# Kernel optimization log

Hardware: AMD Instinct MI355X
Metric: run time of the kernel (lower is better)

The kernel has to match this reference:

```python
import jax, jax.numpy as jnp
import numpy as np
from jax import lax

RADIUS = 51  # radius=50 bumped to odd in __init__
# cv2.getGaussianKernel(51, 0): sigma = 0.3*((ksize-1)*0.5 - 1) + 0.8 = 8.0
SIGMA = 0.3 * ((RADIUS - 1) * 0.5 - 1) + 0.8
WEIGHT = 0.5
THRESHOLD = 10.0


def _gaussian_kernel2d():
    x = np.arange(RADIUS, dtype=np.float64) - (RADIUS - 1) / 2.0
    g = np.exp(-(x ** 2) / (2.0 * SIGMA ** 2))
    g = g / g.sum()
    k2d = np.outer(g, g)
    return jnp.asarray(k2d, dtype=jnp.float32)


def filter2d(img, kernel):
    # img: (b, h, w, c); kernel: (k, k); reflect pad + depthwise conv, VALID
    k = kernel.shape[-1]
    c = img.shape[-1]
    p = k // 2
    imgp = jnp.pad(img, [(0, 0), (p, p), (p, p), (0, 0)], mode='reflect')
    kern = jnp.tile(kernel[:, :, None, None].astype(img.dtype), (1, 1, 1, c))  # HWIO, I=1
    return lax.conv_general_dilated(
        imgp, kern, window_strides=(1, 1), padding='VALID',
        dimension_numbers=('NHWC', 'HWIO', 'NHWC'), feature_group_count=c)


def setup_inputs() -> dict:
    key = jax.random.key(0)
    img = jax.random.uniform(key, (16, 512, 512, 3), dtype=jnp.float32)
    kernel = _gaussian_kernel2d()
    return {"img": img, "kernel": kernel}


def reference(img, kernel):
    blur = filter2d(img, kernel)
    residual = img - blur
    mask = (jnp.abs(residual) * 255.0 > THRESHOLD).astype(img.dtype)
    soft_mask = filter2d(mask, kernel)
    sharp = jnp.clip(img + WEIGHT * residual, 0.0, 1.0)
    return soft_mask * sharp + (1.0 - soft_mask) * img
```

## Files before the change

### kernel.cpp

```cpp
#include <hip/hip_runtime.h>
#include <hip/hip_fp16.h>

#define BB 16
#define HH 512
#define ROWLEN 1536
#define KK 51
#define RR 25

__device__ __forceinline__ int sq(int q) { return q ^ ((q >> 3) & 7); }

__global__ void k_weights(const float* __restrict__ k2d, float* __restrict__ g,
                          __half2* __restrict__ g2) {
    int i = threadIdx.x;
    if (i < KK) {
        float s = 0.f;
        for (int j = 0; j < KK; ++j) s += k2d[i * KK + j];
        g[i] = s;
        g2[i] = __float2half2_rn(s);
    }
}

#define PSTR 576
template<bool U8>
__global__ __launch_bounds__(256, 4) void k_hconv(const void* __restrict__ srcv,
                                                  __half* __restrict__ dst,
                                                  __half* __restrict__ imgh,
                                                  const __half2* __restrict__ g2src) {
    __shared__ __align__(16) __half2 pl[6 * PSTR];
    const int t = threadIdx.x;
    const int row0 = blockIdx.x * 4;

    __half2 gw2[KK];
    #pragma unroll
    for (int i = 0; i < KK; ++i) gw2[i] = g2src[i];

    const int rp = t >> 7;
    const int l  = t & 127;
    const size_t rb0 = (size_t)(row0 + 2 * rp) * ROWLEN;
    const size_t rb1 = rb0 + ROWLEN;

    {
        float f0[12], f1[12];
        if (U8) {
            const unsigned char* sa = (const unsigned char*)srcv + rb0 + 12 * l;
            const unsigned char* sb = (const unsigned char*)srcv + rb1 + 12 * l;
            unsigned int wa[3], wb[3];
            wa[0] = *(const unsigned int*)(sa);
            wa[1] = *(const unsigned int*)(sa + 4);
            wa[2] = *(const unsigned int*)(sa + 8);
            wb[0] = *(const unsigned int*)(sb);
            wb[1] = *(const unsigned int*)(sb + 4);
            wb[2] = *(const unsigned int*)(sb + 8);
            #pragma unroll
            for (int k = 0; k < 12; ++k) {
                f0[k] = (float)((wa[k >> 2] >> ((k & 3) * 8)) & 0xffu);
                f1[k] = (float)((wb[k >> 2] >> ((k & 3) * 8)) & 0xffu);
            }
        } else {
            const float* sfa = (const float*)srcv + rb0 + 12 * l;
            const float* sfb = (const float*)srcv + rb1 + 12 * l;
            *(float4*)&f0[0] = *(const float4*)(sfa);
            *(float4*)&f0[4] = *(const float4*)(sfa + 4);
            *(float4*)&f0[8] = *(const float4*)(sfa + 8);
            *(float4*)&f1[0] = *(const float4*)(sfb);
            *(float4*)&f1[4] = *(const float4*)(sfb + 4);
            *(float4*)&f1[8] = *(const float4*)(sfb + 8);
            union { __half h[12]; uint2 u2[3]; } pa, pb2;
            #pragma unroll
            for (int k = 0; k < 12; ++k) {
                pa.h[k]  = __float2half_rn(f0[k]);
                pb2.h[k] = __float2half_rn(f1[k]);
            }
            uint2* ipa = (uint2*)(imgh + rb0 + 12 * l);
            uint2* ipb = (uint2*)(imgh + rb1 + 12 * l);
            ipa[0] = pa.u2[0];  ipa[1] = pa.u2[1];  ipa[2] = pa.u2[2];
            ipb[0] = pb2.u2[0]; ipb[1] = pb2.u2[1]; ipb[2] = pb2.u2[2];
        }
        const int q = sq(7 + l);
        #pragma unroll
        for (int c = 0; c < 3; ++c) {
            union { __half2 h2[4]; uint4 u; } o;
            #pragma unroll
            for (int i = 0; i < 4; ++i)
                o.h2[i] = __halves2half2(__float2half_rn(f0[3 * i + c]),
                                         __float2half_rn(f1[3 * i + c]));
            *(uint4*)&pl[(rp * 3 + c) * PSTR + 4 * q] = o.u;
        }
    }
    __syncthreads();

    #pragma unroll
    for (int it = 0; it < 2; ++it) {
        const int item = t + it * 256;
        if (item < 300) {
            const int p = item / 50, k = item % 50;
            int ed, es;
            if (k < 25) { const int j = k + 1;  ed = 28 - j;  es = 28 + j; }
            else        { const int j = k - 24; ed = 539 + j; es = 539 - j; }
            __half2* pb = &pl[p * PSTR];
            pb[4 * sq(ed >> 2) + (ed & 3)] = pb[4 * sq(es >> 2) + (es & 3)];
        }
    }
    __syncthreads();

    __half2 acc2[3][4];
    const __half2 z2 = __float2half2_rn(0.f);
    #pragma unroll
    for (int c = 0; c < 3; ++c)
        #pragma unroll
        for (int a = 0; a < 4; ++a) acc2[c][a] = z2;

    #pragma unroll
    for (int c = 0; c < 3; ++c) {
        const __half2* pb = &pl[(rp * 3 + c) * PSTR];
        #pragma unroll
        for (int v = 0; v < 15; ++v) {
            union { uint4 u; __half2 h2[4]; } v4;
            v4.u = *(const uint4*)&pb[4 * sq(l + v)];
            #pragma unroll
            for (int mm = 0; mm < 4; ++mm) {
                const __half2 val = v4.h2[mm];
                #pragma unroll
                for (int a = 0; a < 4; ++a) {
                    const int jj = 4 * v + mm - a - 3;
                    if (jj >= 0 && jj < KK)
                        acc2[c][a] = __hfma2(gw2[jj], val, acc2[c][a]);
                }
            }
        }
    }

    {
        union { __half h[12]; uint2 u2[3]; } pk;
        #pragma unroll
        for (int a = 0; a < 4; ++a)
            #pragma unroll
            for (int c = 0; c < 3; ++c) pk.h[3 * a + c] = __low2half(acc2[c][a]);
        uint2* dp = (uint2*)(dst + rb0 + 12 * l);
        dp[0] = pk.u2[0]; dp[1] = pk.u2[1]; dp[2] = pk.u2[2];
    }
    {
        union { __half h[12]; uint2 u2[3]; } pk;
        #pragma unroll
        for (int a = 0; a < 4; ++a)
            #pragma unroll
            for (int c = 0; c < 3; ++c) pk.h[3 * a + c] = __high2half(acc2[c][a]);
        uint2* dp = (uint2*)(dst + rb1 + 12 * l);
        dp[0] = pk.u2[0]; dp[1] = pk.u2[1]; dp[2] = pk.u2[2];
    }
}

#define HC 128
#define VROWS 178
#define HSTR 72

template<int MODE>
__global__ __launch_bounds__(256) void k_vconv(const __half* __restrict__ src,
                                               const __half* __restrict__ imgh,
                                               __half* __restrict__ sharp16,
                                               float* __restrict__ outp,
                                               unsigned char* __restrict__ mask8,
                                               const __half2* __restrict__ g2src) {
    __shared__ __align__(16) __half tile[VROWS * HSTR];
    const int t  = threadIdx.x;
    const int cg = t & 7;
    const int rg = t >> 3;
    const int bid = blockIdx.x;
    const int wcB = bid % 24;
    const int hB  = (bid / 24) & 3;
    const int b   = bid / 96;
    const int wc0 = wcB * 64;
    const int h0  = hB * HC;

    __half2 gw2[KK];
    #pragma unroll
    for (int i = 0; i < KK; ++i) gw2[i] = g2src[i];

    const size_t imgbase = (size_t)b * HH * ROWLEN;

    #pragma unroll
    for (int i = 0; i < 6; ++i) {
        const int m = t + 256 * i;
        if (m < VROWS * 8) {
            const int r = m >> 3, cc = m & 7;
            int hs = h0 - RR + r;
            hs = hs < 0 ? -hs : hs;
            hs = hs > 511 ? 1022 - hs : hs;
            *(uint4*)&tile[r * HSTR + 8 * cc] =
                *(const uint4*)&src[imgbase + (size_t)hs * ROWLEN + wc0 + 8 * cc];
        }
    }
    __syncthreads();

    __half2 acc[4][4];
    const __half2 z2 = __float2half2_rn(0.f);
    #pragma unroll
    for (int a = 0; a < 4; ++a)
        #pragma unroll
        for (int p = 0; p < 4; ++p) acc[a][p] = z2;

    const __half* base = &tile[(rg * 4) * HSTR + 8 * cg];
    #pragma unroll
    for (int jj = 0; jj < 54; ++jj) {
        const uint4 raw = *(const uint4*)(base + jj * HSTR);
        union { uint4 u; __half2 h2[4]; } v; v.u = raw;
        #pragma unroll
        for (int a = 0; a < 4; ++a) {
            const int tap = jj - a;
            if (tap >= 0 && tap < KK) {
                acc[a][0] = __hfma2(gw2[tap], v.h2[0], acc[a][0]);
                acc[a][1] = __hfma2(gw2[tap], v.h2[1], acc[a][1]);
                acc[a][2] = __hfma2(gw2[tap], v.h2[2], acc[a][2]);
                acc[a][3] = __hfma2(gw2[tap], v.h2[3], acc[a][3]);
            }
        }
    }

    #pragma unroll
    for (int a = 0; a < 4; ++a) {
        const int hh = h0 + rg * 4 + a;
        const size_t idx = imgbase + (size_t)hh * ROWLEN + wc0 + 8 * cg;
        union { uint4 u; __half2 h2[4]; } xl;
        xl.u = *(const uint4*)&imgh[idx];
        float xv[8], bv[8];
        #pragma unroll
        for (int p = 0; p < 4; ++p) {
            const float2 xf = __half22float2(xl.h2[p]);
            const float2 bf = __half22float2(acc[a][p]);
            xv[2*p] = xf.x; xv[2*p+1] = xf.y;
            bv[2*p] = bf.x; bv[2*p+1] = bf.y;
        }
        if (MODE == 0) {
            union { __half h[8]; uint4 u; } sh;
            unsigned int mwlo = 0, mwhi = 0;
            #pragma unroll
            for (int m = 0; m < 8; ++m) {
                const float x = xv[m];
                const float res = x - bv[m];
                sh.h[m] = __float2half_rn(fminf(fmaxf(x + 0.5f * res, 0.f), 1.f));
                const unsigned int bit = (fabsf(res) * 255.0f > 10.0f) ? 1u : 0u;
                if (m < 4) mwlo |= bit << (8 * m); else mwhi |= bit << (8 * (m - 4));
            }
            *(uint4*)&sharp16[idx] = sh.u;
            uint2 mo; mo.x = mwlo; mo.y = mwhi;
            *(uint2*)&mask8[idx] = mo;
        } else {
            union { uint4 u; __half2 h2[4]; } sl;
            sl.u = *(const uint4*)&sharp16[idx];
            float ov[8];
            #pragma unroll
            for (int p = 0; p < 4; ++p) {
                const float2 sf = __half22float2(sl.h2[p]);
                ov[2*p]   = xv[2*p]   + bv[2*p]   * (sf.x - xv[2*p]);
                ov[2*p+1] = xv[2*p+1] + bv[2*p+1] * (sf.y - xv[2*p+1]);
            }
            float4 o0, o1;
            o0.x = ov[0]; o0.y = ov[1]; o0.z = ov[2]; o0.w = ov[3];
            o1.x = ov[4]; o1.y = ov[5]; o1.z = ov[6]; o1.w = ov[7];
            *(float4*)&outp[idx]     = o0;
            *(float4*)&outp[idx + 4] = o1;
        }
    }
}

extern "C" void kernel_launch(void* const* d_in, const int* in_sizes, int n_in,
                              void* d_out, int out_size, void* d_ws, size_t ws_size,
                              hipStream_t stream) {
    (void)in_sizes; (void)n_in; (void)out_size; (void)ws_size;
    const float* img = (const float*)d_in[0];
    const float* k2d = (const float*)d_in[1];
    float* out = (float*)d_out;

    const size_t NPX = (size_t)BB * HH * ROWLEN;
    char* ws = (char*)d_ws;
    float* g = (float*)ws;
    __half2* g2 = (__half2*)(ws + 256);
    __half* tbuf = (__half*)(ws + 512);
    unsigned char* mask8 = (unsigned char*)(ws + 512 + NPX * 2);
    __half* sharp16 = (__half*)(ws + 512 + NPX * 2 + NPX);
    __half* imgh    = (__half*)(ws + 512 + NPX * 2 + NPX + NPX * 2);

    const int nhblk = BB * HH / 4;
    const int nvblk = BB * 4 * 24;

    k_weights<<<1, 64, 0, stream>>>(k2d, g, g2);
    k_hconv<false><<<nhblk, 256, 0, stream>>>((const void*)img, tbuf, imgh, g2);
    k_vconv<0><<<nvblk, 256, 0, stream>>>(tbuf, imgh, sharp16, out, mask8, g2);
    k_hconv<true><<<nhblk, 256, 0, stream>>>((const void*)mask8, tbuf, imgh, g2);
    k_vconv<1><<<nvblk, 256, 0, stream>>>(tbuf, imgh, sharp16, out, mask8, g2);
}
```

Before: 95.91 us.

## Bit-pack mask, drop sharp buffer, recompute blur in final vertical pass

The first vertical pass now writes only a bit-packed mask (one byte per 8 pixels) rather than an fp16 sharp image plus a byte mask. The final vertical pass keeps both horizontal intermediates and recomputes the blur vertically to derive sharp on the fly. The aim is to cut global memory traffic for the mask and the sharp buffer. Nontemporal loads and stores are used for the input and output, and the mask hconv expands bits directly into fp16. The cost is a second 51-tap vertical convolution and double the shared memory in the final kernel, which may reduce occupancy.

```diff
diff --git a/kernel.cpp b/kernel.cpp
--- a/kernel.cpp
+++ b/kernel.cpp
@@ -6,6 +6,8 @@
 #define ROWLEN 1536
 #define KK 51
 #define RR 25
+typedef unsigned long long u64;
+typedef float nt4 __attribute__((ext_vector_type(4)));
 
 __device__ __forceinline__ int sq(int q) { return q ^ ((q >> 3) & 7); }
 
@@ -21,7 +23,7 @@
 }
 
 #define PSTR 576
-template<bool U8>
+template<bool MASKP>
 __global__ __launch_bounds__(256, 4) void k_hconv(const void* __restrict__ srcv,
                                                   __half* __restrict__ dst,
                                                   __half* __restrict__ imgh,
@@ -40,31 +42,37 @@
     const size_t rb1 = rb0 + ROWLEN;
 
     {
-        float f0[12], f1[12];
-        if (U8) {
-            const unsigned char* sa = (const unsigned char*)srcv + rb0 + 12 * l;
-            const unsigned char* sb = (const unsigned char*)srcv + rb1 + 12 * l;
-            unsigned int wa[3], wb[3];
-            wa[0] = *(const unsigned int*)(sa);
-            wa[1] = *(const unsigned int*)(sa + 4);
-            wa[2] = *(const unsigned int*)(sa + 8);
-            wb[0] = *(const unsigned int*)(sb);
-            wb[1] = *(const unsigned int*)(sb + 4);
-            wb[2] = *(const unsigned int*)(sb + 8);
-            #pragma unroll
-            for (int k = 0; k < 12; ++k) {
-                f0[k] = (float)((wa[k >> 2] >> ((k & 3) * 8)) & 0xffu);
-                f1[k] = (float)((wb[k >> 2] >> ((k & 3) * 8)) & 0xffu);
+        const int q = sq(7 + l);
+        if (MASKP) {
+            const unsigned int* mw = (const unsigned int*)srcv;
+            const size_t wr0 = (size_t)(row0 + 2 * rp) * 48;
+            const int pos = 12 * l, w0i = pos >> 5, sh = pos & 31;
+            const u64 winA = ((u64)mw[wr0 + w0i + 1] << 32) | mw[wr0 + w0i];
+            const u64 winB = ((u64)mw[wr0 + 48 + w0i + 1] << 32) | mw[wr0 + 48 + w0i];
+            const unsigned bA = (unsigned)(winA >> sh) & 0xFFFu;
+            const unsigned bB = (unsigned)(winB >> sh) & 0xFFFu;
+            const __half hz = __float2half_rn(0.f), ho = __float2half_rn(1.f);
+            #pragma unroll
+            for (int c = 0; c < 3; ++c) {
+                union { __half2 h2[4]; uint4 u; } o;
+                #pragma unroll
+                for (int i = 0; i < 4; ++i) {
+                    const int k = 3 * i + c;
+                    o.h2[i] = __halves2half2((bA >> k) & 1 ? ho : hz,
+                                             (bB >> k) & 1 ? ho : hz);
+                }
+                *(uint4*)&pl[(rp * 3 + c) * PSTR + 4 * q] = o.u;
             }
         } else {
+            float f0[12], f1[12];
             const float* sfa = (const float*)srcv + rb0 + 12 * l;
             const float* sfb = (const float*)srcv + rb1 + 12 * l;
-            *(float4*)&f0[0] = *(const float4*)(sfa);
-            *(float4*)&f0[4] = *(const float4*)(sfa + 4);
-            *(float4*)&f0[8] = *(const float4*)(sfa + 8);
-            *(float4*)&f1[0] = *(const float4*)(sfb);
-            *(float4*)&f1[4] = *(const float4*)(sfb + 4);
-            *(float4*)&f1[8] = *(const float4*)(sfb + 8);
+            *(nt4*)&f0[0] = __builtin_nontemporal_load((const nt4*)(sfa));
+            *(nt4*)&f0[4] = __builtin_nontemporal_load((const nt4*)(sfa + 4));
+            *(nt4*)&f0[8] = __builtin_nontemporal_load((const nt4*)(sfa + 8));
+            *(nt4*)&f1[0] = __builtin_nontemporal_load((const nt4*)(sfb));
+            *(nt4*)&f1[4] = __builtin_nontemporal_load((const nt4*)(sfb + 4));
+            *(nt4*)&f1[8] = __builtin_nontemporal_load((const nt4*)(sfb + 8));
             union { __half h[12]; uint2 u2[3]; } pa, pb2;
             #pragma unroll
             for (int k = 0; k < 12; ++k) {
@@ -75,16 +83,14 @@
             uint2* ipb = (uint2*)(imgh + rb1 + 12 * l);
             ipa[0] = pa.u2[0];  ipa[1] = pa.u2[1];  ipa[2] = pa.u2[2];
             ipb[0] = pb2.u2[0]; ipb[1] = pb2.u2[1]; ipb[2] = pb2.u2[2];
-        }
-        const int q = sq(7 + l);
-        #pragma unroll
-        for (int c = 0; c < 3; ++c) {
-            union { __half2 h2[4]; uint4 u; } o;
-            #pragma unroll
-            for (int i = 0; i < 4; ++i)
-                o.h2[i] = __halves2half2(__float2half_rn(f0[3 * i + c]),
-                                         __float2half_rn(f1[3 * i + c]));
-            *(uint4*)&pl[(rp * 3 + c) * PSTR + 4 * q] = o.u;
+            #pragma unroll
+            for (int c = 0; c < 3; ++c) {
+                union { __half2 h2[4]; uint4 u; } o;
+                #pragma unroll
+                for (int i = 0; i < 4; ++i)
+                    o.h2[i] = __halves2half2(pa.h[3 * i + c], pb2.h[3 * i + c]);
+                *(uint4*)&pl[(rp * 3 + c) * PSTR + 4 * q] = o.u;
+            }
         }
     }
     __syncthreads();
@@ -154,12 +160,9 @@
 #define VROWS 178
 #define HSTR 72
 
-template<int MODE>
-__global__ __launch_bounds__(256) void k_vconv(const __half* __restrict__ src,
+__global__ __launch_bounds__(256) void k_vmask(const __half* __restrict__ src,
                                                const __half* __restrict__ imgh,
-                                               __half* __restrict__ sharp16,
-                                               float* __restrict__ outp,
-                                               unsigned char* __restrict__ mask8,
+                                               unsigned char* __restrict__ maskp,
                                                const __half2* __restrict__ g2src) {
     __shared__ __align__(16) __half tile[VROWS * HSTR];
     const int t  = threadIdx.x;
@@ -222,44 +225,118 @@
         const size_t idx = imgbase + (size_t)hh * ROWLEN + wc0 + 8 * cg;
         union { uint4 u; __half2 h2[4]; } xl;
         xl.u = *(const uint4*)&imgh[idx];
-        float xv[8], bv[8];
+        unsigned int byte = 0;
         #pragma unroll
         for (int p = 0; p < 4; ++p) {
             const float2 xf = __half22float2(xl.h2[p]);
             const float2 bf = __half22float2(acc[a][p]);
-            xv[2*p] = xf.x; xv[2*p+1] = xf.y;
-            bv[2*p] = bf.x; bv[2*p+1] = bf.y;
-        }
-        if (MODE == 0) {
-            union { __half h[8]; uint4 u; } sh;
-            unsigned int mwlo = 0, mwhi = 0;
-            #pragma unroll
-            for (int m = 0; m < 8; ++m) {
-                const float x = xv[m];
-                const float res = x - bv[m];
-                sh.h[m] = __float2half_rn(fminf(fmaxf(x + 0.5f * res, 0.f), 1.f));
-                const unsigned int bit = (fabsf(res) * 255.0f > 10.0f) ? 1u : 0u;
-                if (m < 4) mwlo |= bit << (8 * m); else mwhi |= bit << (8 * (m - 4));
-            }
-            *(uint4*)&sharp16[idx] = sh.u;
-            uint2 mo; mo.x = mwlo; mo.y = mwhi;
-            *(uint2*)&mask8[idx] = mo;
-        } else {
-            union { uint4 u; __half2 h2[4]; } sl;
-            sl.u = *(const uint4*)&sharp16[idx];
-            float ov[8];
-            #pragma unroll
-            for (int p = 0; p < 4; ++p) {
-                const float2 sf = __half22float2(sl.h2[p]);
-                ov[2*p]   = xv[2*p]   + bv[2*p]   * (sf.x - xv[2*p]);
-                ov[2*p+1] = xv[2*p+1] + bv[2*p+1] * (sf.y - xv[2*p+1]);
-            }
-            float4 o0, o1;
-            o0.x = ov[0]; o0.y = ov[1]; o0.z = ov[2]; o0.w = ov[3];
-            o1.x = ov[4]; o1.y = ov[5]; o1.z = ov[6]; o1.w = ov[7];
-            *(float4*)&outp[idx]     = o0;
-            *(float4*)&outp[idx + 4] = o1;
-        }
+            if (fabsf(xf.x - bf.x) * 255.0f > 10.0f) byte |= 1u << (2 * p);
+            if (fabsf(xf.y - bf.y) * 255.0f > 10.0f) byte |= 1u << (2 * p + 1);
+        }
+        maskp[((size_t)b * HH + hh) * 192 + (wc0 >> 3) + cg] = (unsigned char)byte;
+    }
+}
+
+__global__ __launch_bounds__(256) void k_vfinal(const __half* __restrict__ srcA,
+                                                const __half* __restrict__ srcB,
+                                                const __half* __restrict__ imgh,
+                                                float* __restrict__ outp,
+                                                const __half2* __restrict__ g2src) {
+    __shared__ __align__(16) __half tileA[VROWS * HSTR];
+    __shared__ __align__(16) __half tileB[VROWS * HSTR];
+    const int t  = threadIdx.x;
+    const int cg = t & 7;
+    const int rg = t >> 3;
+    const int bid = blockIdx.x;
+    const int wcB = bid % 24;
+    const int hB  = (bid / 24) & 3;
+    const int b   = bid / 96;
+    const int wc0 = wcB * 64;
+    const int h0  = hB * HC;
+
+    __half2 gw2[KK];
+    #pragma unroll
+    for (int i = 0; i < KK; ++i) gw2[i] = g2src[i];
+
+    const size_t imgbase = (size_t)b * HH * ROWLEN;
+
+    #pragma unroll
+    for (int i = 0; i < 6; ++i) {
+        const int m = t + 256 * i;
+        if (m < VROWS * 8) {
+            const int r = m >> 3, cc = m & 7;
+            int hs = h0 - RR + r;
+            hs = hs < 0 ? -hs : hs;
+            hs = hs > 511 ? 1022 - hs : hs;
+            const size_t ga = imgbase + (size_t)hs * ROWLEN + wc0 + 8 * cc;
+            *(uint4*)&tileA[r * HSTR + 8 * cc] = *(const uint4*)&srcA[ga];
+            *(uint4*)&tileB[r * HSTR + 8 * cc] = *(const uint4*)&srcB[ga];
+        }
+    }
+    __syncthreads();
+
+    const __half2 z2 = __float2half2_rn(0.f);
+    __half2 accB[4][4], accS[4][4];
+    #pragma unroll
+    for (int a = 0; a < 4; ++a)
+        #pragma unroll
+        for (int p = 0; p < 4; ++p) { accB[a][p] = z2; accS[a][p] = z2; }
+
+    const __half* baseA = &tileA[(rg * 4) * HSTR + 8 * cg];
+    #pragma unroll
+    for (int jj = 0; jj < 54; ++jj) {
+        union { uint4 u; __half2 h2[4]; } v;
+        v.u = *(const uint4*)(baseA + jj * HSTR);
+        #pragma unroll
+        for (int a = 0; a < 4; ++a) {
+            const int tap = jj - a;
+            if (tap >= 0 && tap < KK) {
+                accB[a][0] = __hfma2(gw2[tap], v.h2[0], accB[a][0]);
+                accB[a][1] = __hfma2(gw2[tap], v.h2[1], accB[a][1]);
+                accB[a][2] = __hfma2(gw2[tap], v.h2[2], accB[a][2]);
+                accB[a][3] = __hfma2(gw2[tap], v.h2[3], accB[a][3]);
+            }
+        }
+    }
+    const __half* baseB = &tileB[(rg * 4) * HSTR + 8 * cg];
+    #pragma unroll
+    for (int jj = 0; jj < 54; ++jj) {
+        union { uint4 u; __half2 h2[4]; } v;
+        v.u = *(const uint4*)(baseB + jj * HSTR);
+        #pragma unroll
+        for (int a = 0; a < 4; ++a) {
+            const int tap = jj - a;
+            if (tap >= 0 && tap < KK) {
+                accS[a][0] = __hfma2(gw2[tap], v.h2[0], accS[a][0]);
+                accS[a][1] = __hfma2(gw2[tap], v.h2[1], accS[a][1]);
+                accS[a][2] = __hfma2(gw2[tap], v.h2[2], accS[a][2]);
+                accS[a][3] = __hfma2(gw2[tap], v.h2[3], accS[a][3]);
+            }
+        }
+    }
+
+    #pragma unroll
+    for (int a = 0; a < 4; ++a) {
+        const int hh = h0 + rg * 4 + a;
+        const size_t idx = imgbase + (size_t)hh * ROWLEN + wc0 + 8 * cg;
+        union { uint4 u; __half2 h2[4]; } xl;
+        xl.u = *(const uint4*)&imgh[idx];
+        float ov[8];
+        #pragma unroll
+        for (int p = 0; p < 4; ++p) {
+            const float2 xf = __half22float2(xl.h2[p]);
+            const float2 bf = __half22float2(accB[a][p]);
+            const float2 sf = __half22float2(accS[a][p]);
+            const float sh0 = fminf(fmaxf(xf.x + 0.5f * (xf.x - bf.x), 0.f), 1.f);
+            const float sh1 = fminf(fmaxf(xf.y + 0.5f * (xf.y - bf.y), 0.f), 1.f);
+            ov[2*p]   = xf.x + sf.x * (sh0 - xf.x);
+            ov[2*p+1] = xf.y + sf.y * (sh1 - xf.y);
+        }
+        nt4 o0, o1;
+        o0.x = ov[0]; o0.y = ov[1]; o0.z = ov[2]; o0.w = ov[3];
+        o1.x = ov[4]; o1.y = ov[5]; o1.z = ov[6]; o1.w = ov[7];
+        __builtin_nontemporal_store(o0, (nt4*)&outp[idx]);
+        __builtin_nontemporal_store(o1, (nt4*)&outp[idx + 4]);
     }
 }
 
@@ -275,17 +352,17 @@
     char* ws = (char*)d_ws;
     float* g = (float*)ws;
     __half2* g2 = (__half2*)(ws + 256);
-    __half* tbuf = (__half*)(ws + 512);
-    unsigned char* mask8 = (unsigned char*)(ws + 512 + NPX * 2);
-    __half* sharp16 = (__half*)(ws + 512 + NPX * 2 + NPX);
-    __half* imgh    = (__half*)(ws + 512 + NPX * 2 + NPX + NPX * 2);
+    __half* tbufA = (__half*)(ws + 512);
+    __half* tbufB = (__half*)(ws + 512 + NPX * 2);
+    __half* imgh  = (__half*)(ws + 512 + NPX * 4);
+    unsigned char* maskp = (unsigned char*)(ws + 512 + NPX * 6);
 
     const int nhblk = BB * HH / 4;
     const int nvblk = BB * 4 * 24;
 
     k_weights<<<1, 64, 0, stream>>>(k2d, g, g2);
-    k_hconv<false><<<nhblk, 256, 0, stream>>>((const void*)img, tbuf, imgh, g2);
-    k_vconv<0><<<nvblk, 256, 0, stream>>>(tbuf, imgh, sharp16, out, mask8, g2);
-    k_hconv<true><<<nhblk, 256, 0, stream>>>((const void*)mask8, tbuf, imgh, g2);
-    k_vconv<1><<<nvblk, 256, 0, stream>>>(tbuf, imgh, sharp16, out, mask8, g2);
-}
+    k_hconv<false><<<nhblk, 256, 0, stream>>>((const void*)img, tbufA, imgh, g2);
+    k_vmask<<<nvblk, 256, 0, stream>>>(tbufA, imgh, maskp, g2);
+    k_hconv<true><<<nhblk, 256, 0, stream>>>((const void*)maskp, tbufB, imgh, g2);
+    k_vfinal<<<nvblk, 256, 0, stream>>>(tbufA, tbufB, imgh, out, g2);
+}
```

New measurement: 109.2 us. +13.8%, slower.
